# Performance work log

Measured on AMD Instinct MI355X. Metric: run time of the kernel, lower is better.

Reference implementation:

```python
import jax, jax.numpy as jnp
import numpy as np

N = 100000   # nodes
E = 1600000  # edges (avg degree 16)
F_IN, H1, H2, H3, C = 500, 200, 100, 40, 3


def setup_inputs() -> dict:
    key = jax.random.key(0)
    ks = jax.random.split(key, 10)
    def w(k, shape, fan_in):
        return jax.random.normal(k, shape, dtype=jnp.float32) / np.sqrt(fan_in)
    return {
        "x": jax.random.normal(ks[0], (N, F_IN), dtype=jnp.float32),
        "edge_index": jax.random.randint(ks[1], (2, E), 0, N, dtype=jnp.int32),
        "W1": w(ks[2], (H1, F_IN), F_IN), "b1": jnp.zeros((H1,), jnp.float32),
        "W1b": w(ks[3], (H2, H1), H1),  "b1b": jnp.zeros((H2,), jnp.float32),
        "W2b": w(ks[4], (H3, H2), H2),  "b2b": jnp.zeros((H3,), jnp.float32),
        "W2": w(ks[5], (C, H3), H3),    "b2": jnp.zeros((C,), jnp.float32),
    }


def _gcn_conv(x, W, b, src, dst, norm_e, n):
    # GCNConv: linear transform, then normalized scatter-add aggregation, then bias
    h = x @ W.T                                   # [N, out]
    msgs = h[src] * norm_e[:, None]               # [E+N, out] gathered, normalized
    out = jax.ops.segment_sum(msgs, dst, num_segments=n)
    return out + b


def reference(x, edge_index, W1, b1, W1b, b1b, W2b, b2b, W2, b2):
    n = x.shape[0]
    loop = jnp.arange(n, dtype=edge_index.dtype)
    src = jnp.concatenate([edge_index[0], loop])  # add self-loops (GCNConv default)
    dst = jnp.concatenate([edge_index[1], loop])
    # symmetric normalization: deg computed on target nodes, norm = d^-1/2[src]*d^-1/2[dst]
    deg = jax.ops.segment_sum(jnp.ones_like(dst, dtype=x.dtype), dst, num_segments=n)
    dinv = jnp.where(deg > 0, jax.lax.rsqrt(deg), 0.0)
    norm_e = dinv[src] * dinv[dst]

    # dropout(p=0.5, training=self.training) is identity at inference
    h = jax.nn.relu(_gcn_conv(x, W1, b1, src, dst, norm_e, n))
    h = jax.nn.relu(_gcn_conv(h, W1b, b1b, src, dst, norm_e, n))
    h = jax.nn.relu(_gcn_conv(h, W2b, b2b, src, dst, norm_e, n))
    return _gcn_conv(h, W2, b2, src, dst, norm_e, n)
```

## Files before the change

kernel.cpp:

```cpp
#include <hip/hip_runtime.h>


#define DEV __device__ __forceinline__

typedef __attribute__((ext_vector_type(8))) short short8;
typedef __attribute__((ext_vector_type(8))) _Float16 f16x8;
typedef __attribute__((ext_vector_type(4))) float f32x4;
typedef __attribute__((ext_vector_type(4))) _Float16 f16x4;

DEV void gload_lds16(const void* g, void* l) {
    __builtin_amdgcn_global_load_lds(
        (const __attribute__((address_space(1))) unsigned int*)g,
        (__attribute__((address_space(3))) unsigned int*)l, 16, 0, 0);
}


__global__ void k_prep(const int* __restrict__ dst, int* __restrict__ cnt,
                       int* __restrict__ rank, int E,
                       const float* __restrict__ W1, unsigned short* __restrict__ wh1,
                       const float* __restrict__ W1b, unsigned short* __restrict__ wh2,
                       unsigned short* __restrict__ wl2,
                       const float* __restrict__ W2b, unsigned short* __restrict__ wh3,
                       unsigned short* __restrict__ wl3) {
    const int SZ1 = 224 * 512, SZ2 = 128 * 256, SZ3 = 64 * 128;
    int i = blockIdx.x * 256 + threadIdx.x;
    if (i < E) {
        rank[i] = atomicAdd(&cnt[dst[i]], 1);
        return;
    }
    i -= E;
    if (i < SZ1) {
        int r = i >> 9, k = i & 511;
        float x = (r < 200 && k < 500) ? W1[r * 500 + k] : 0.f;
        wh1[i] = __builtin_bit_cast(unsigned short, (_Float16)x);
        return;
    }
    i -= SZ1;
    if (i < SZ2) {
        int r = i >> 8, k = i & 255;
        float x = (r < 100 && k < 200) ? W1b[r * 200 + k] : 0.f;
        _Float16 h = (_Float16)x;
        _Float16 l = (_Float16)((x - (float)h) * 2048.0f);
        wh2[i] = __builtin_bit_cast(unsigned short, h);
        wl2[i] = __builtin_bit_cast(unsigned short, l);
        return;
    }
    i -= SZ2;
    if (i < SZ3) {
        int r = i >> 7, k = i & 127;
        float x = (r < 40 && k < 100) ? W2b[r * 100 + k] : 0.f;
        _Float16 h = (_Float16)x;
        _Float16 l = (_Float16)((x - (float)h) * 2048.0f);
        wh3[i] = __builtin_bit_cast(unsigned short, h);
        wl3[i] = __builtin_bit_cast(unsigned short, l);
    }
}


__global__ void k_scan1(const int* __restrict__ cnt, int* __restrict__ row_start,
                        int* __restrict__ partial, float* __restrict__ dinv, int n) {
    __shared__ int sdata[256];
    int base = blockIdx.x * 1024;
    int t = threadIdx.x;
    int v[4]; int sum = 0;
#pragma unroll
    for (int j = 0; j < 4; ++j) {
        int idx = base + t * 4 + j;
        v[j] = (idx < n) ? (cnt[idx] + 1) : 0;
        if (idx < n) dinv[idx] = rsqrtf((float)v[j]);
        sum += v[j];
    }
    sdata[t] = sum;
    __syncthreads();
    for (int off = 1; off < 256; off <<= 1) {
        int x = (t >= off) ? sdata[t - off] : 0;
        __syncthreads();
        sdata[t] += x;
        __syncthreads();
    }
    int excl = sdata[t] - sum;
#pragma unroll
    for (int j = 0; j < 4; ++j) {
        int idx = base + t * 4 + j;
        if (idx < n) row_start[idx] = excl;
        excl += v[j];
    }
    if (t == 255) partial[blockIdx.x] = sdata[255];
}

__global__ void k_scan2(int* __restrict__ partial, int nb) {
    __shared__ int s[128];
    int t = threadIdx.x;
    int v = (t < nb) ? partial[t] : 0;
    s[t] = v;
    __syncthreads();
    for (int off = 1; off < 128; off <<= 1) {
        int x = (t >= off) ? s[t - off] : 0;
        __syncthreads();
        s[t] += x;
        __syncthreads();
    }
    if (t < nb) partial[t] = s[t] - v;
}

__global__ void k_scan3(int* __restrict__ row_start, const int* __restrict__ partial,
                        int n, int total) {
    int i = blockIdx.x * 256 + threadIdx.x;
    if (i < n) row_start[i] += partial[i >> 10];
    if (i == 0) row_start[n] = total;
}


struct A8 { f32x4 lo, hi; };

template <int NFC, int KPH, int NPH, int HILO, int MODE, int DOFILL, typename AT>
__global__ __launch_bounds__(512, 4)
void gemm_res(const AT* __restrict__ A, int lda, int M, int K,
              const unsigned short* __restrict__ Wh,
              const unsigned short* __restrict__ Wl,
              const float* __restrict__ dinv,
              _Float16* __restrict__ H16, int ldh, int Nout,
              const int* __restrict__ fsrc, const int* __restrict__ fdst,
              const int* __restrict__ frows, const int* __restrict__ fcnt,
              const int* __restrict__ frank, int* __restrict__ fcsr, int fE, int fN) {
    constexpr int NPAD = NFC * 16;
    constexpr int KP   = KPH * NPH;
    constexpr int CHH  = NPAD * KPH / 8;
    constexpr int CHT  = CHH * (1 + HILO);
    constexpr int NIT  = (CHT + 511) / 512;
    constexpr int SB   = NPAD * 64;
    constexpr int HB   = CHH * 16;
    constexpr int SPP  = KPH / 32;
    constexpr int NS   = SPP * NPH;
    constexpr int D    = 2;
    __shared__ char lds[CHT * 16];

    const int tid  = threadIdx.x;
    const int wv   = tid >> 6;
    const int lane = tid & 63;
    const int lr   = lane & 15;
    const int kq   = lane >> 4;
    const int m0   = blockIdx.y * 128;
    const int col0 = blockIdx.x * NPAD;

    if constexpr (DOFILL) {
        int total = fE + fN;
        int nb    = gridDim.y;
        int per   = (total + nb - 1) / nb;
        int base  = blockIdx.y * per;
        int end   = base + per; if (end > total) end = total;
        for (int i = base + tid; i < end; i += 512) {
            int s, pos;
            if (i < fE) {
                s = fsrc[i];
                pos = frows[fdst[i]] + frank[i];
            } else {
                s = i - fE;
                pos = frows[s] + fcnt[s];
            }
            fcsr[pos] = s;
        }
    }

    const unsigned short* WhB = Wh + (size_t)col0 * KP;
    const unsigned short* WlB = Wl + (size_t)col0 * KP;

    auto stageW = [&](int p) {
#pragma unroll
        for (int i = 0; i < NIT; ++i) {
            int c = tid + i * 512;
            if ((CHT % 512 == 0) || (c < CHT)) {
                int h  = (HILO && c >= CHH) ? 1 : 0;
                int cc = c - h * CHH;
                int st = cc / (NPAD * 4);
                int rm = cc - st * (NPAD * 4);
                int r  = rm >> 2;
                int sl = rm & 3;
                int gs = sl ^ (r & 3);
                const unsigned short* gp = (h ? WlB : WhB)
                    + (size_t)r * KP + p * KPH + st * 32 + gs * 8;
                gload_lds16(gp, lds + (size_t)c * 16);
            }
        }
    };

    int arow = m0 + wv * 16 + lr;
    if (arow >= M) arow = M - 1;
    const AT* Arow = A + (size_t)arow * lda;

    auto loadA32 = [&](int s) -> A8 {
        A8 o;
        int kb = s * 32 + kq * 8;
        if (kb + 8 <= K) {
            const float* ap = (const float*)Arow + kb;
            o.lo = *(const f32x4*)ap;
            o.hi = *(const f32x4*)(ap + 4);
        } else {
#pragma unroll
            for (int i = 0; i < 4; ++i) {
                int k0 = kb + i, k1 = kb + 4 + i;
                o.lo[i] = (k0 < K) ? (float)Arow[k0] : 0.f;
                o.hi[i] = (k1 < K) ? (float)Arow[k1] : 0.f;
            }
        }
        return o;
    };
    auto loadA16 = [&](int s) -> short8 {
        int kb = s * 32 + kq * 8;
        if (kb + 8 <= K) return *(const short8*)((const unsigned short*)Arow + kb);
        short8 o;
        const unsigned short* ap = (const unsigned short*)Arow;
#pragma unroll
        for (int i = 0; i < 8; ++i) o[i] = (kb + i < K) ? (short)ap[kb + i] : (short)0;
        return o;
    };
    auto cvtA = [&](const A8& a) -> f16x8 {
        f16x8 o;
#pragma unroll
        for (int i = 0; i < 4; ++i) {
            o[i]     = (_Float16)a.lo[i];
            o[4 + i] = (_Float16)a.hi[i];
        }
        return o;
    };

    stageW(0);
    A8 ab[D]; short8 hb[D];
#pragma unroll
    for (int p = 0; p < D; ++p) {
        if (p < NS) {
            if constexpr (MODE == 0) ab[p] = loadA32(p);
            else                     hb[p] = loadA16(p);
        }
    }

    f32x4 ac[NFC], al[NFC];
#pragma unroll
    for (int f = 0; f < NFC; ++f) {
        ac[f] = (f32x4){0.f, 0.f, 0.f, 0.f};
        al[f] = (f32x4){0.f, 0.f, 0.f, 0.f};
    }

    __syncthreads();

    const int ro = lr * 64 + ((kq ^ (lr & 3)) << 4);

#pragma unroll
    for (int p = 0; p < NPH; ++p) {
#pragma unroll
        for (int sl = 0; sl < SPP; ++sl) {
            const int s = p * SPP + sl;
            f16x8 a0;
            if constexpr (MODE == 0) a0 = cvtA(ab[s % D]);
            else                     a0 = __builtin_bit_cast(f16x8, hb[s % D]);

            if (s + D < NS) {
                if constexpr (MODE == 0) ab[s % D] = loadA32(s + D);
                else                     hb[s % D] = loadA16(s + D);
            }

            const char* bb = lds + sl * SB;
#pragma unroll
            for (int f = 0; f < NFC; ++f) {
                f16x8 bh = __builtin_bit_cast(f16x8, *(const short8*)(bb + f * 1024 + ro));
                ac[f] = __builtin_amdgcn_mfma_f32_16x16x32_f16(a0, bh, ac[f], 0, 0, 0);
                if constexpr (HILO) {
                    f16x8 bl = __builtin_bit_cast(f16x8, *(const short8*)(bb + HB + f * 1024 + ro));
                    al[f] = __builtin_amdgcn_mfma_f32_16x16x32_f16(a0, bl, al[f], 0, 0, 0);
                }
            }
        }
        if (p + 1 < NPH) {
            __syncthreads();
            stageW(p + 1);
            __syncthreads();
        }
    }

    const int rbase = m0 + wv * 16 + kq * 4;
    float dv[4];
#pragma unroll
    for (int j = 0; j < 4; ++j) {
        int row = rbase + j;
        dv[j] = (row < M) ? dinv[row] : 0.f;
    }
#pragma unroll
    for (int f = 0; f < NFC; ++f) {
        int col = col0 + f * 16 + lr;
        if (col >= Nout) continue;
#pragma unroll
        for (int j = 0; j < 4; ++j) {
            int row = rbase + j;
            if (row >= M) continue;
            float v = ac[f][j];
            if constexpr (HILO) v += al[f][j] * (1.0f / 2048.0f);
            H16[(size_t)row * ldh + col] = (_Float16)(v * dv[j]);
        }
    }
}


template <int F, int VEC, bool RELU>
__global__ __launch_bounds__(256)
void agg_f16(const _Float16* __restrict__ h, const int* __restrict__ row_start,
             const int* __restrict__ csr_src, const float* __restrict__ dinv,
             const float* __restrict__ bias, _Float16* __restrict__ out, int n,
             int ldo) {
    constexpr int LPN = F / VEC;
    int gid  = blockIdx.x * 256 + threadIdx.x;
    int node = gid / LPN;
    int fi   = gid - node * LPN;
    if (node >= n) return;
    int f = fi * VEC;
    const _Float16* hf = h + f;

    f32x4 acc0 = {0.f, 0.f, 0.f, 0.f};
    f32x4 acc1 = {0.f, 0.f, 0.f, 0.f};

    auto addv = [&](const _Float16* p) {
        if constexpr (VEC == 8) {
            f16x8 v = *(const f16x8*)p;
            f16x4 vl, vh;
#pragma unroll
            for (int j = 0; j < 4; ++j) { vl[j] = v[j]; vh[j] = v[4 + j]; }
            acc0 += __builtin_convertvector(vl, f32x4);
            acc1 += __builtin_convertvector(vh, f32x4);
        } else {
            f16x4 v = *(const f16x4*)p;
            acc0 += __builtin_convertvector(v, f32x4);
        }
    };

    int e0 = row_start[node], e1 = row_start[node + 1];
    int e = e0;
    for (; e + 4 <= e1; e += 4) {
        int s0 = csr_src[e + 0];
        int s1 = csr_src[e + 1];
        int s2 = csr_src[e + 2];
        int s3 = csr_src[e + 3];
        const _Float16* p0 = &hf[(size_t)s0 * F];
        const _Float16* p1 = &hf[(size_t)s1 * F];
        const _Float16* p2 = &hf[(size_t)s2 * F];
        const _Float16* p3 = &hf[(size_t)s3 * F];
        addv(p0); addv(p1); addv(p2); addv(p3);
    }
    for (; e < e1; ++e) addv(&hf[(size_t)csr_src[e] * F]);

    float dn = dinv[node];
    if constexpr (VEC == 8) {
        f32x4 b0 = *(const f32x4*)&bias[f];
        f32x4 b1 = *(const f32x4*)&bias[f + 4];
        acc0 = acc0 * dn + b0;
        acc1 = acc1 * dn + b1;
        if (RELU) {
#pragma unroll
            for (int j = 0; j < 4; ++j) { acc0[j] = fmaxf(acc0[j], 0.f); acc1[j] = fmaxf(acc1[j], 0.f); }
        }
        f16x8 o;
#pragma unroll
        for (int j = 0; j < 4; ++j) { o[j] = (_Float16)acc0[j]; o[4 + j] = (_Float16)acc1[j]; }
        *(f16x8*)&out[(size_t)node * ldo + f] = o;
    } else {
        f32x4 b4 = *(const f32x4*)&bias[f];
        acc0 = acc0 * dn + b4;
        if (RELU) {
#pragma unroll
            for (int j = 0; j < 4; ++j) acc0[j] = fmaxf(acc0[j], 0.f);
        }
        f16x4 o;
#pragma unroll
        for (int j = 0; j < 4; ++j) o[j] = (_Float16)acc0[j];
        *(f16x4*)&out[(size_t)node * ldo + f] = o;
    }
}


__global__ void gemm_small(const _Float16* __restrict__ A, const float* __restrict__ B,
                           const float* __restrict__ dinv, float* __restrict__ C,
                           int M, int K) {
    int m = blockIdx.x * 256 + threadIdx.x;
    if (m >= M) return;
    float a0 = 0.f, a1 = 0.f, a2 = 0.f;
    for (int k = 0; k < K; ++k) {
        float a = (float)A[(size_t)m * K + k];
        a0 += a * B[0 * K + k];
        a1 += a * B[1 * K + k];
        a2 += a * B[2 * K + k];
    }
    float dv = dinv[m];
    C[(size_t)m * 3 + 0] = a0 * dv;
    C[(size_t)m * 3 + 1] = a1 * dv;
    C[(size_t)m * 3 + 2] = a2 * dv;
}

__global__ void agg_f3(const float* __restrict__ h, const int* __restrict__ row_start,
                       const int* __restrict__ csr_src, const float* __restrict__ dinv,
                       const float* __restrict__ bias, float* __restrict__ out, int n) {
    int i = blockIdx.x * 256 + threadIdx.x;
    if (i >= n * 3) return;
    int node = i / 3;
    int f = i - node * 3;
    float acc = 0.f;
    int e1 = row_start[node + 1];
    for (int e = row_start[node]; e < e1; ++e) {
        int s = csr_src[e];
        acc += h[(size_t)s * 3 + f];
    }
    out[i] = acc * dinv[node] + bias[f];
}


extern "C" void kernel_launch(void* const* d_in, const int* in_sizes, int n_in,
                              void* d_out, int out_size, void* d_ws, size_t ws_size,
                              hipStream_t stream) {
    const float* x   = (const float*)d_in[0];
    const int*   ei  = (const int*)d_in[1];
    const float* W1  = (const float*)d_in[2];
    const float* b1  = (const float*)d_in[3];
    const float* W1b = (const float*)d_in[4];
    const float* b1b = (const float*)d_in[5];
    const float* W2b = (const float*)d_in[6];
    const float* b2b = (const float*)d_in[7];
    const float* W2  = (const float*)d_in[8];
    const float* b2  = (const float*)d_in[9];
    float* out = (float*)d_out;

    const int F_IN = 500, H1 = 200, H2 = 100, H3 = 40;
    const int N = in_sizes[0] / F_IN;
    const int E = in_sizes[1] / 2;
    const int* src = ei;
    const int* dst = ei + E;

    size_t off = 0;
    auto alloc = [&](size_t bytes) -> void* {
        void* p = (char*)d_ws + off;
        off += (bytes + 255) & ~(size_t)255;
        return p;
    };
    int*   cnt       = (int*)  alloc((size_t)N * 4);
    int*   row_start = (int*)  alloc((size_t)(N + 1) * 4);
    int*   rank      = (int*)  alloc((size_t)E * 4);
    int*   partial   = (int*)  alloc(128 * 4);
    float* dinv      = (float*)alloc((size_t)N * 4);
    int*   csr_src   = (int*)  alloc((size_t)(E + N) * 4);
    unsigned short* wh1 = (unsigned short*)alloc(224 * 512 * 2);
    unsigned short* wh2 = (unsigned short*)alloc(128 * 256 * 2);
    unsigned short* wl2 = (unsigned short*)alloc(128 * 256 * 2);
    unsigned short* wh3 = (unsigned short*)alloc( 64 * 128 * 2);
    unsigned short* wl3 = (unsigned short*)alloc( 64 * 128 * 2);
    _Float16* h16   = (_Float16*)alloc((size_t)N * H1 * 2);
    _Float16* act16 = (_Float16*)alloc((size_t)N * H1 * 2);
    float*    bufC  = (float*)   alloc((size_t)N * 3 * 4);

    int gN = (N + 255) / 256;
    int nb = (N + 1023) / 1024;

    hipMemsetAsync(cnt, 0, (size_t)N * 4, stream);
    {
        int total = E + 224 * 512 + 128 * 256 + 64 * 128;
        k_prep<<<(total + 255) / 256, 256, 0, stream>>>(dst, cnt, rank, E,
                                                        W1, wh1, W1b, wh2, wl2,
                                                        W2b, wh3, wl3);
    }
    k_scan1<<<nb, 256, 0, stream>>>(cnt, row_start, partial, dinv, N);
    k_scan2<<<1, 128, 0, stream>>>(partial, nb);
    k_scan3<<<gN, 256, 0, stream>>>(row_start, partial, N, E + N);

    const int gR = (N + 127) / 128;

    gemm_res<14, 128, 4, 0, 0, 1, float><<<dim3(1, gR), 512, 0, stream>>>(
        x, F_IN, N, F_IN, wh1, wh1, dinv, h16, H1, H1,
        src, dst, row_start, cnt, rank, csr_src, E, N);
    {
        long long thr = (long long)N * 25;
        agg_f16<200, 8, true><<<(int)((thr + 255) / 256), 256, 0, stream>>>(
            h16, row_start, csr_src, dinv, b1, act16, N, 200);
    }
    gemm_res<8, 128, 2, 1, 1, 0, _Float16><<<dim3(1, gR), 512, 0, stream>>>(
        act16, 200, N, H1, wh2, wl2, dinv, h16, H2, H2,
        nullptr, nullptr, nullptr, nullptr, nullptr, nullptr, 0, 0);
    {
        long long thr = (long long)N * 25;
        agg_f16<100, 4, true><<<(int)((thr + 255) / 256), 256, 0, stream>>>(
            h16, row_start, csr_src, dinv, b1b, act16, N, 112);
    }
    gemm_res<4, 128, 1, 1, 1, 0, _Float16><<<dim3(1, gR), 512, 0, stream>>>(
        act16, 112, N, H2, wh3, wl3, dinv, h16, H3, H3,
        nullptr, nullptr, nullptr, nullptr, nullptr, nullptr, 0, 0);
    {
        long long thr = (long long)N * 5;
        agg_f16<40, 8, true><<<(int)((thr + 255) / 256), 256, 0, stream>>>(
            h16, row_start, csr_src, dinv, b2b, act16, N, 40);
    }
    gemm_small<<<(N + 255) / 256, 256, 0, stream>>>(act16, W2, dinv, bufC, N, H3);
    agg_f3<<<(N * 3 + 255) / 256, 256, 0, stream>>>(bufC, row_start, csr_src, dinv,
                                                    b2, out, N);
}
```

Before: 499.5 us.

## Pre-convert x to padded fp16, register-stage weights, unroll aggregation by eight

Input x is converted once into a zero-padded fp16 buffer of width 512 inside the prep kernel, so the first GEMM reads fp16 rows without bounds checks or in-loop conversion. Weight staging switches from direct global-to-LDS loads to prefetching the next phase into registers and storing to LDS after the barrier. The aggregation gather loop gains an 8-way unrolled path. The conversion adds an extra full pass over x (read fp32, write fp16) that costs roughly as much traffic as the first GEMM saves, and the removed K bounds checks now rely on padded leading dimensions.

```diff
diff --git a/kernel.cpp b/kernel.cpp
--- a/kernel.cpp
+++ b/kernel.cpp
@@ -17,30 +17,45 @@
 
 __global__ void k_prep(const int* __restrict__ dst, int* __restrict__ cnt,
                        int* __restrict__ rank, int E,
+                       const float* __restrict__ x, _Float16* __restrict__ x16, int N,
                        const float* __restrict__ W1, unsigned short* __restrict__ wh1,
                        const float* __restrict__ W1b, unsigned short* __restrict__ wh2,
                        unsigned short* __restrict__ wl2,
                        const float* __restrict__ W2b, unsigned short* __restrict__ wh3,
                        unsigned short* __restrict__ wl3) {
     const int SZ1 = 224 * 512, SZ2 = 128 * 256, SZ3 = 64 * 128;
+    const int SZX = N * 64;
     int i = blockIdx.x * 256 + threadIdx.x;
     if (i < E) {
         rank[i] = atomicAdd(&cnt[dst[i]], 1);
         return;
     }
     i -= E;
+    if (i < SZX) {
+        int r = i >> 6, c = i & 63;
+        int k0 = c * 8;
+        f16x8 o;
+#pragma unroll
+        for (int j = 0; j < 8; ++j) {
+            int k = k0 + j;
+            o[j] = (k < 500) ? (_Float16)x[(size_t)r * 500 + k] : (_Float16)0.f;
+        }
+        *(f16x8*)&x16[(size_t)r * 512 + k0] = o;
+        return;
+    }
+    i -= SZX;
     if (i < SZ1) {
         int r = i >> 9, k = i & 511;
-        float x = (r < 200 && k < 500) ? W1[r * 500 + k] : 0.f;
-        wh1[i] = __builtin_bit_cast(unsigned short, (_Float16)x);
+        float v = (r < 200 && k < 500) ? W1[r * 500 + k] : 0.f;
+        wh1[i] = __builtin_bit_cast(unsigned short, (_Float16)v);
         return;
     }
     i -= SZ1;
     if (i < SZ2) {
         int r = i >> 8, k = i & 255;
-        float x = (r < 100 && k < 200) ? W1b[r * 200 + k] : 0.f;
-        _Float16 h = (_Float16)x;
-        _Float16 l = (_Float16)((x - (float)h) * 2048.0f);
+        float v = (r < 100 && k < 200) ? W1b[r * 200 + k] : 0.f;
+        _Float16 h = (_Float16)v;
+        _Float16 l = (_Float16)((v - (float)h) * 2048.0f);
         wh2[i] = __builtin_bit_cast(unsigned short, h);
         wl2[i] = __builtin_bit_cast(unsigned short, l);
         return;
@@ -48,9 +63,9 @@
     i -= SZ2;
     if (i < SZ3) {
         int r = i >> 7, k = i & 127;
-        float x = (r < 40 && k < 100) ? W2b[r * 100 + k] : 0.f;
-        _Float16 h = (_Float16)x;
-        _Float16 l = (_Float16)((x - (float)h) * 2048.0f);
+        float v = (r < 40 && k < 100) ? W2b[r * 100 + k] : 0.f;
+        _Float16 h = (_Float16)v;
+        _Float16 l = (_Float16)((v - (float)h) * 2048.0f);
         wh3[i] = __builtin_bit_cast(unsigned short, h);
         wl3[i] = __builtin_bit_cast(unsigned short, l);
     }
@@ -111,11 +126,9 @@
 }
 
 
-struct A8 { f32x4 lo, hi; };
-
-template <int NFC, int KPH, int NPH, int HILO, int MODE, int DOFILL, typename AT>
+template <int NFC, int KPH, int NPH, int HILO, int DOFILL>
 __global__ __launch_bounds__(512, 4)
-void gemm_res(const AT* __restrict__ A, int lda, int M, int K,
+void gemm_res(const _Float16* __restrict__ A, int lda, int M, int K,
               const unsigned short* __restrict__ Wh,
               const unsigned short* __restrict__ Wl,
               const float* __restrict__ dinv,
@@ -127,7 +140,7 @@
     constexpr int KP   = KPH * NPH;
     constexpr int CHH  = NPAD * KPH / 8;
     constexpr int CHT  = CHH * (1 + HILO);
-    constexpr int NIT  = (CHT + 511) / 512;
+    constexpr int NIT  = CHT / 512;
     constexpr int SB   = NPAD * 64;
     constexpr int HB   = CHH * 16;
     constexpr int SPP  = KPH / 32;
@@ -165,74 +178,37 @@
     const unsigned short* WhB = Wh + (size_t)col0 * KP;
     const unsigned short* WlB = Wl + (size_t)col0 * KP;
 
-    auto stageW = [&](int p) {
-#pragma unroll
-        for (int i = 0; i < NIT; ++i) {
-            int c = tid + i * 512;
-            if ((CHT % 512 == 0) || (c < CHT)) {
-                int h  = (HILO && c >= CHH) ? 1 : 0;
-                int cc = c - h * CHH;
-                int st = cc / (NPAD * 4);
-                int rm = cc - st * (NPAD * 4);
-                int r  = rm >> 2;
-                int sl = rm & 3;
-                int gs = sl ^ (r & 3);
-                const unsigned short* gp = (h ? WlB : WhB)
-                    + (size_t)r * KP + p * KPH + st * 32 + gs * 8;
-                gload_lds16(gp, lds + (size_t)c * 16);
-            }
-        }
-    };
+    const unsigned short* gpb[NIT];
+    int ldo_[NIT];
+#pragma unroll
+    for (int i = 0; i < NIT; ++i) {
+        int c  = tid + i * 512;
+        int h  = (HILO && c >= CHH) ? 1 : 0;
+        int cc = c - h * CHH;
+        int st = cc / (NPAD * 4);
+        int rm = cc - st * (NPAD * 4);
+        int r  = rm >> 2;
+        int sl = rm & 3;
+        int gs = sl ^ (r & 3);
+        gpb[i] = (h ? WlB : WhB) + (size_t)r * KP + st * 32 + gs * 8;
+        ldo_[i] = c * 16;
+    }
+
+#pragma unroll
+    for (int i = 0; i < NIT; ++i) gload_lds16(gpb[i], lds + ldo_[i]);
 
     int arow = m0 + wv * 16 + lr;
     if (arow >= M) arow = M - 1;
-    const AT* Arow = A + (size_t)arow * lda;
-
-    auto loadA32 = [&](int s) -> A8 {
-        A8 o;
-        int kb = s * 32 + kq * 8;
-        if (kb + 8 <= K) {
-            const float* ap = (const float*)Arow + kb;
-            o.lo = *(const f32x4*)ap;
-            o.hi = *(const f32x4*)(ap + 4);
-        } else {
-#pragma unroll
-            for (int i = 0; i < 4; ++i) {
-                int k0 = kb + i, k1 = kb + 4 + i;
-                o.lo[i] = (k0 < K) ? (float)Arow[k0] : 0.f;
-                o.hi[i] = (k1 < K) ? (float)Arow[k1] : 0.f;
-            }
-        }
-        return o;
+    const _Float16* Arow = A + (size_t)arow * lda;
+
+    auto loadA = [&](int s) -> short8 {
+        return *(const short8*)((const unsigned short*)Arow + s * 32 + kq * 8);
     };
-    auto loadA16 = [&](int s) -> short8 {
-        int kb = s * 32 + kq * 8;
-        if (kb + 8 <= K) return *(const short8*)((const unsigned short*)Arow + kb);
-        short8 o;
-        const unsigned short* ap = (const unsigned short*)Arow;
-#pragma unroll
-        for (int i = 0; i < 8; ++i) o[i] = (kb + i < K) ? (short)ap[kb + i] : (short)0;
-        return o;
-    };
-    auto cvtA = [&](const A8& a) -> f16x8 {
-        f16x8 o;
-#pragma unroll
-        for (int i = 0; i < 4; ++i) {
-            o[i]     = (_Float16)a.lo[i];
-            o[4 + i] = (_Float16)a.hi[i];
-        }
-        return o;
-    };
-
-    stageW(0);
-    A8 ab[D]; short8 hb[D];
-#pragma unroll
-    for (int p = 0; p < D; ++p) {
-        if (p < NS) {
-            if constexpr (MODE == 0) ab[p] = loadA32(p);
-            else                     hb[p] = loadA16(p);
-        }
-    }
+
+    short8 hb[D];
+#pragma unroll
+    for (int p = 0; p < D; ++p)
+        if (p < NS) hb[p] = loadA(p);
 
     f32x4 ac[NFC], al[NFC];
 #pragma unroll
@@ -245,19 +221,20 @@
 
     const int ro = lr * 64 + ((kq ^ (lr & 3)) << 4);
 
+    uint4 wreg[NIT > 0 ? NIT : 1];
+
 #pragma unroll
     for (int p = 0; p < NPH; ++p) {
+        if (p + 1 < NPH) {
+#pragma unroll
+            for (int i = 0; i < NIT; ++i)
+                wreg[i] = *(const uint4*)(gpb[i] + (size_t)(p + 1) * KPH);
+        }
 #pragma unroll
         for (int sl = 0; sl < SPP; ++sl) {
             const int s = p * SPP + sl;
-            f16x8 a0;
-            if constexpr (MODE == 0) a0 = cvtA(ab[s % D]);
-            else                     a0 = __builtin_bit_cast(f16x8, hb[s % D]);
-
-            if (s + D < NS) {
-                if constexpr (MODE == 0) ab[s % D] = loadA32(s + D);
-                else                     hb[s % D] = loadA16(s + D);
-            }
+            f16x8 a0 = __builtin_bit_cast(f16x8, hb[s % D]);
+            if (s + D < NS) hb[s % D] = loadA(s + D);
 
             const char* bb = lds + sl * SB;
 #pragma unroll
@@ -272,7 +249,8 @@
         }
         if (p + 1 < NPH) {
             __syncthreads();
-            stageW(p + 1);
+#pragma unroll
+            for (int i = 0; i < NIT; ++i) *(uint4*)(lds + ldo_[i]) = wreg[i];
             __syncthreads();
         }
     }
@@ -333,11 +311,25 @@
 
     int e0 = row_start[node], e1 = row_start[node + 1];
     int e = e0;
+    for (; e + 8 <= e1; e += 8) {
+        int s0 = csr_src[e + 0], s1 = csr_src[e + 1];
+        int s2 = csr_src[e + 2], s3 = csr_src[e + 3];
+        int s4 = csr_src[e + 4], s5 = csr_src[e + 5];
+        int s6 = csr_src[e + 6], s7 = csr_src[e + 7];
+        const _Float16* p0 = &hf[(size_t)s0 * F];
+        const _Float16* p1 = &hf[(size_t)s1 * F];
+        const _Float16* p2 = &hf[(size_t)s2 * F];
+        const _Float16* p3 = &hf[(size_t)s3 * F];
+        const _Float16* p4 = &hf[(size_t)s4 * F];
+        const _Float16* p5 = &hf[(size_t)s5 * F];
+        const _Float16* p6 = &hf[(size_t)s6 * F];
+        const _Float16* p7 = &hf[(size_t)s7 * F];
+        addv(p0); addv(p1); addv(p2); addv(p3);
+        addv(p4); addv(p5); addv(p6); addv(p7);
+    }
     for (; e + 4 <= e1; e += 4) {
-        int s0 = csr_src[e + 0];
-        int s1 = csr_src[e + 1];
-        int s2 = csr_src[e + 2];
-        int s3 = csr_src[e + 3];
+        int s0 = csr_src[e + 0], s1 = csr_src[e + 1];
+        int s2 = csr_src[e + 2], s3 = csr_src[e + 3];
         const _Float16* p0 = &hf[(size_t)s0 * F];
         const _Float16* p1 = &hf[(size_t)s1 * F];
         const _Float16* p2 = &hf[(size_t)s2 * F];
@@ -448,19 +440,20 @@
     unsigned short* wl2 = (unsigned short*)alloc(128 * 256 * 2);
     unsigned short* wh3 = (unsigned short*)alloc( 64 * 128 * 2);
     unsigned short* wl3 = (unsigned short*)alloc( 64 * 128 * 2);
-    _Float16* h16   = (_Float16*)alloc((size_t)N * H1 * 2);
-    _Float16* act16 = (_Float16*)alloc((size_t)N * H1 * 2);
-    float*    bufC  = (float*)   alloc((size_t)N * 3 * 4);
+    _Float16* x16  = (_Float16*)alloc((size_t)N * 512 * 2);
+    _Float16* h16  = (_Float16*)alloc((size_t)N * H1 * 2);
+    float*    bufC = (float*)   alloc((size_t)N * 3 * 4);
+    _Float16* act16 = x16;
 
     int gN = (N + 255) / 256;
     int nb = (N + 1023) / 1024;
 
     hipMemsetAsync(cnt, 0, (size_t)N * 4, stream);
     {
-        int total = E + 224 * 512 + 128 * 256 + 64 * 128;
-        k_prep<<<(total + 255) / 256, 256, 0, stream>>>(dst, cnt, rank, E,
-                                                        W1, wh1, W1b, wh2, wl2,
-                                                        W2b, wh3, wl3);
+        long long total = (long long)E + (long long)N * 64
+                        + 224 * 512 + 128 * 256 + 64 * 128;
+        k_prep<<<(int)((total + 255) / 256), 256, 0, stream>>>(
+            dst, cnt, rank, E, x, x16, N, W1, wh1, W1b, wh2, wl2, W2b, wh3, wl3);
     }
     k_scan1<<<nb, 256, 0, stream>>>(cnt, row_start, partial, dinv, N);
     k_scan2<<<1, 128, 0, stream>>>(partial, nb);
@@ -468,15 +461,15 @@
 
     const int gR = (N + 127) / 128;
 
-    gemm_res<14, 128, 4, 0, 0, 1, float><<<dim3(1, gR), 512, 0, stream>>>(
-        x, F_IN, N, F_IN, wh1, wh1, dinv, h16, H1, H1,
+    gemm_res<14, 128, 4, 0, 1><<<dim3(1, gR), 512, 0, stream>>>(
+        x16, 512, N, 512, wh1, wh1, dinv, h16, H1, H1,
         src, dst, row_start, cnt, rank, csr_src, E, N);
     {
         long long thr = (long long)N * 25;
         agg_f16<200, 8, true><<<(int)((thr + 255) / 256), 256, 0, stream>>>(
             h16, row_start, csr_src, dinv, b1, act16, N, 200);
     }
-    gemm_res<8, 128, 2, 1, 1, 0, _Float16><<<dim3(1, gR), 512, 0, stream>>>(
+    gemm_res<8, 128, 2, 1, 0><<<dim3(1, gR), 512, 0, stream>>>(
         act16, 200, N, H1, wh2, wl2, dinv, h16, H2, H2,
         nullptr, nullptr, nullptr, nullptr, nullptr, nullptr, 0, 0);
     {
@@ -484,7 +477,7 @@
         agg_f16<100, 4, true><<<(int)((thr + 255) / 256), 256, 0, stream>>>(
             h16, row_start, csr_src, dinv, b1b, act16, N, 112);
     }
-    gemm_res<4, 128, 1, 1, 1, 0, _Float16><<<dim3(1, gR), 512, 0, stream>>>(
+    gemm_res<4, 128, 1, 1, 0><<<dim3(1, gR), 512, 0, stream>>>(
         act16, 112, N, H2, wh3, wl3, dinv, h16, H3, H3,
         nullptr, nullptr, nullptr, nullptr, nullptr, nullptr, 0, 0);
     {
```

Measured after the change: 644.9 us. +29.1%, slower.
